# Optimization experiments

Hardware: AMD Instinct MI355X
Metric: run time of the kernel (lower is better)

The kernel has to match this reference:

```python
import jax, jax.numpy as jnp
import numpy as np

ALPHA = 0.2
NOISE_STD = 0.05
I, H, O, R, S, G = 3, 2048, 2, 2, 4, 7
B, T = 32, 512


def _proxies(wi, unitwi, m, n, unitm, unitn, wo, h0, unith0, bias, gb, uv, sup):
    # gb: (G,H) gaussian basis, uv: (1,H) unit vector, sup: (S,H) support masks
    def comb(p, up):  # p: (K,S,G), up: (K,S,1) -> (K,H)
        return jnp.sum((jnp.einsum('ksg,gh->ksh', p, gb) + up * uv) * sup, axis=1)

    wi_full = comb(wi, unitwi)                                          # (I,H)
    m_rec = comb(m, unitm).T                                            # (H,R)
    n_rec = comb(n, unitn).T                                            # (H,R)
    wo_full = jnp.sum(jnp.einsum('osg,gh->osh', wo, gb) * sup, axis=1).T  # (H,O)
    h0_full = jnp.sum((h0 @ gb) * sup, axis=0) + jnp.sum((unith0 * uv) * sup, axis=0)  # (H,)
    bias_full = jnp.sum((bias * uv) * sup, axis=0)                      # (H,)
    w_rec = m_rec @ n_rec.T                                             # (H,H)
    return wi_full, wo_full, w_rec, h0_full, bias_full


def setup_inputs() -> dict:
    key = jax.random.key(0)
    ks = jax.random.split(key, 16)
    sc = 1.0 / np.sqrt(G)
    sup = np.zeros((S, H), dtype=np.float32)
    l = H // S
    for i in range(S):
        sup[i, l * i:l * (i + 1)] = 1.0
    return {
        'input': jax.random.normal(ks[0], (B, T, I), jnp.float32),
        'noise': jax.random.normal(ks[1], (B, T, H), jnp.float32),
        'wi': jax.random.normal(ks[2], (I, S, G), jnp.float32) * sc,
        'unitwi': jax.random.normal(ks[3], (I, S, 1), jnp.float32) * sc,
        'm': jax.random.normal(ks[4], (R, S, G), jnp.float32) * sc,
        'n': jax.random.normal(ks[5], (R, S, G), jnp.float32) * sc,
        'unitm': jax.random.normal(ks[6], (R, S, 1), jnp.float32) * sc,
        'unitn': jax.random.normal(ks[7], (R, S, 1), jnp.float32) * sc,
        'wo': jax.random.normal(ks[8], (O, S, G), jnp.float32) * sc,
        'h0': jax.random.normal(ks[9], (S, G), jnp.float32) * sc,
        'unith0': jax.random.normal(ks[10], (S, 1), jnp.float32) * sc,
        'bias': jax.random.normal(ks[11], (S, 1), jnp.float32) * 0.01,
        'gaussian_basis': jax.random.normal(ks[12], (G, H), jnp.float32),
        'unit_vector': jnp.ones((1, H), jnp.float32),
        'supports': jnp.asarray(sup),
    }


def reference(input, noise, wi, unitwi, m, n, unitm, unitn, wo, h0, unith0, bias,
              gaussian_basis, unit_vector, supports):
    wi_full, wo_full, w_rec, h0_full, bias_full = _proxies(
        wi, unitwi, m, n, unitm, unitn, wo, h0, unith0, bias,
        gaussian_basis, unit_vector, supports)
    batch = input.shape[0]
    h0b = jnp.broadcast_to(h0_full, (batch, h0_full.shape[0]))  # (B,H)

    def step(h, xs):
        x_t, z_t = xs                       # (B,I), (B,H)
        r = jnp.tanh(h)
        h = h + bias_full + NOISE_STD * z_t + ALPHA * (-h + r @ w_rec.T + x_t @ wi_full)
        r = jnp.tanh(h)
        return h, (r @ wo_full, h)

    _, (out, traj) = jax.lax.scan(step, h0b,
                                  (jnp.swapaxes(input, 0, 1), jnp.swapaxes(noise, 0, 1)))
    return jnp.swapaxes(out, 0, 1), jnp.swapaxes(traj, 0, 1)  # (B,T,O), (B,T,H)
```

## Files before the change

### kernel.cpp

```cpp
#include <hip/hip_runtime.h>

typedef float v2f __attribute__((ext_vector_type(2)));

constexpr int I_N = 3, H_N = 2048, O_N = 2, S_N = 4, G_N = 7;
constexpr int B_N = 32, T_N = 512;
constexpr int TPB = 512;
constexpr int EPT = H_N / TPB;
constexpr float ALPHA_C = 0.2f;
constexpr float NSTD_C = 0.05f;
constexpr float TWO_LOG2E = 2.885390081777927f;

__device__ __forceinline__ float fast_tanh(float x) {
  float e = __builtin_amdgcn_exp2f(x * TWO_LOG2E);
  return fmaf(-2.0f, __builtin_amdgcn_rcpf(e + 1.0f), 1.0f);
}

#define DPP_ADD(x, ctrl, rmask)                                                \
  x += __int_as_float(__builtin_amdgcn_update_dpp(                             \
      0, __float_as_int(x), (ctrl), (rmask), 0xf, true))

__device__ __forceinline__ float wave_sum63(float x) {
  DPP_ADD(x, 0x111, 0xf);
  DPP_ADD(x, 0x112, 0xf);
  DPP_ADD(x, 0x114, 0xf);
  DPP_ADD(x, 0x118, 0xf);
  DPP_ADD(x, 0x142, 0xa);
  DPP_ADD(x, 0x143, 0xc);
  return x;
}

__device__ __forceinline__ float rfl(float v) {
  return __int_as_float(__builtin_amdgcn_readfirstlane(__float_as_int(v)));
}

__global__ __launch_bounds__(256) void wo_precomp(
    const float* __restrict__ wo, const float* __restrict__ gb,
    const float* __restrict__ sup, float2* __restrict__ ws2) {
  const int h = blockIdx.x * 256 + threadIdx.x;
  const int s = h >> 9;
  const float sv = sup[s * H_N + h];
  float c0 = 0.f, c1 = 0.f;
#pragma unroll
  for (int g = 0; g < G_N; ++g) {
    const float gv = gb[g * H_N + h];
    c0 = fmaf(wo[(0 * S_N + s) * G_N + g], gv, c0);
    c1 = fmaf(wo[(1 * S_N + s) * G_N + g], gv, c1);
  }
  ws2[h] = make_float2(c0 * sv, c1 * sv);
}

__global__ __launch_bounds__(256) void out_proj(
    const float* __restrict__ traj, const float2* __restrict__ ws2,
    float* __restrict__ out) {
  const int blk = blockIdx.x;
  const int tid = threadIdx.x;
  const int lane = tid & 63;
  const int wave = tid >> 6;
  const int hb = tid * 8;

  __shared__ float2 red[4];

  const float* tp = traj + (size_t)blk * H_N + hb;
  float4 t0 = *(const float4*)tp;
  float4 t1 = *(const float4*)(tp + 4);
  float2 c[8];
#pragma unroll
  for (int e = 0; e < 8; ++e) c[e] = ws2[hb + e];

  float hv[8] = {t0.x, t0.y, t0.z, t0.w, t1.x, t1.y, t1.z, t1.w};
  float p0 = 0.f, p1 = 0.f;
#pragma unroll
  for (int e = 0; e < 8; ++e) {
    const float rv = fast_tanh(hv[e]);
    p0 = fmaf(rv, c[e].x, p0);
    p1 = fmaf(rv, c[e].y, p1);
  }
  p0 = wave_sum63(p0);
  p1 = wave_sum63(p1);
  if (lane == 63) red[wave] = make_float2(p0, p1);
  __syncthreads();
  if (tid == 0) {
    float o0 = 0.f, o1 = 0.f;
#pragma unroll
    for (int w = 0; w < 4; ++w) {
      o0 += red[w].x;
      o1 += red[w].y;
    }
    ((float2*)out)[blk] = make_float2(o0, o1);
  }
}

__global__ __launch_bounds__(TPB) void rnn_fused(
    const float* __restrict__ input,
    const float* __restrict__ noise,
    const float* __restrict__ wi,
    const float* __restrict__ unitwi,
    const float* __restrict__ m_,
    const float* __restrict__ n_,
    const float* __restrict__ unitm,
    const float* __restrict__ unitn,
    const float* __restrict__ h0,
    const float* __restrict__ unith0,
    const float* __restrict__ bias,
    const float* __restrict__ gb,
    const float* __restrict__ uv,
    const float* __restrict__ sup,
    float* __restrict__ traj) {
  const int tid = threadIdx.x;
  const int lane = tid & 63;
  const int wave = tid >> 6;
  const int b = blockIdx.x;
  const int hbase = tid * EPT;
  const int s = hbase >> 9;

  __shared__ float2 parts[2][16];
  __shared__ float4 xs4[T_N];

  float cn0[EPT], cn1[EPT], cm0[EPT], cm1[EPT];
  float cw0[EPT], cw1[EPT], cw2[EPT];
  float cb[EPT], hh_[EPT], r[EPT];

  for (int e = 0; e < EPT; ++e) {
    const int hh = hbase + e;
    float gbh[G_N];
#pragma unroll
    for (int g = 0; g < G_N; ++g) gbh[g] = gb[g * H_N + hh];
    const float uvh = uv[hh];
    const float sv = sup[s * H_N + hh];

    auto comb = [&](const float* p, const float* up, int k) {
      float acc = up[k * S_N + s] * uvh;
#pragma unroll
      for (int g = 0; g < G_N; ++g)
        acc = fmaf(p[(k * S_N + s) * G_N + g], gbh[g], acc);
      return acc * sv;
    };

    cn0[e] = comb(n_, unitn, 0);
    cn1[e] = comb(n_, unitn, 1);
    cm0[e] = ALPHA_C * comb(m_, unitm, 0);
    cm1[e] = ALPHA_C * comb(m_, unitm, 1);
    cw0[e] = ALPHA_C * comb(wi, unitwi, 0);
    cw1[e] = ALPHA_C * comb(wi, unitwi, 1);
    cw2[e] = ALPHA_C * comb(wi, unitwi, 2);
    cb[e] = bias[s] * uvh * sv;
    hh_[e] = comb(h0, unith0, 0);
    r[e] = fast_tanh(hh_[e]);
  }

  v2f cnp[EPT];
  v2f cm0p[2], cm1p[2], cw0p[2], cw1p[2], cw2p[2], cbp[2];
#pragma unroll
  for (int e = 0; e < EPT; ++e) cnp[e] = (v2f){cn0[e], cn1[e]};
#pragma unroll
  for (int p2 = 0; p2 < 2; ++p2) {
    cm0p[p2] = (v2f){cm0[2 * p2], cm0[2 * p2 + 1]};
    cm1p[p2] = (v2f){cm1[2 * p2], cm1[2 * p2 + 1]};
    cw0p[p2] = (v2f){cw0[2 * p2], cw0[2 * p2 + 1]};
    cw1p[p2] = (v2f){cw1[2 * p2], cw1[2 * p2 + 1]};
    cw2p[p2] = (v2f){cw2[2 * p2], cw2[2 * p2 + 1]};
    cbp[p2] = (v2f){cb[2 * p2], cb[2 * p2 + 1]};
  }
  v2f h01 = (v2f){hh_[0], hh_[1]};
  v2f h23 = (v2f){hh_[2], hh_[3]};

  const float* zp = noise + ((size_t)b * T_N) * H_N + hbase;
  const float* xp = input + ((size_t)b * T_N) * I_N;
  float* tp = traj + ((size_t)b * T_N) * H_N + hbase;

  {
    const float* xq = xp + tid * I_N;
    xs4[tid] = make_float4(xq[0], xq[1], xq[2], 0.0f);
  }
  if (tid < 16) parts[tid >> 3][8 + (tid & 7)] = make_float2(0.f, 0.f);

  float4 zr0 = *(const float4*)zp;
  float4 zr1 = *(const float4*)(zp + 1 * (size_t)H_N);
  float4 zr2 = *(const float4*)(zp + 2 * (size_t)H_N);
  float4 zr3 = *(const float4*)(zp + 3 * (size_t)H_N);
  float4 zr4 = *(const float4*)(zp + 4 * (size_t)H_N);
  float4 zr5 = *(const float4*)(zp + 5 * (size_t)H_N);
  float4 zr6 = *(const float4*)(zp + 6 * (size_t)H_N);
  float4 zr7 = *(const float4*)(zp + 7 * (size_t)H_N);

  __builtin_amdgcn_s_waitcnt(0xC07F);
  __builtin_amdgcn_s_barrier();
  __asm__ volatile("" ::: "memory");

  float4 xv = xs4[0];

  auto body = [&](int t, int pb, float4& zslot) {
    const float4 z0 = zslot;
    const int tz = (t + 8 < T_N) ? t + 8 : T_N - 1;
    float4 zn = *(const float4*)(zp + (size_t)tz * H_N);
    const int tx = (t + 1 < T_N) ? t + 1 : T_N - 1;
    float4 xn = xs4[tx];

    v2f z01 = (v2f){z0.x, z0.y}, z23 = (v2f){z0.z, z0.w};
    v2f pre01 = cbp[0];
    pre01 += NSTD_C * z01;
    pre01 += xv.x * cw0p[0];
    pre01 += xv.y * cw1p[0];
    pre01 += xv.z * cw2p[0];
    v2f pre23 = cbp[1];
    pre23 += NSTD_C * z23;
    pre23 += xv.x * cw0p[1];
    pre23 += xv.y * cw1p[1];
    pre23 += xv.z * cw2p[1];

    v2f accA = (v2f){0.f, 0.f};
#pragma unroll
    for (int e = 0; e < EPT; ++e) {
      v2f rr = (v2f){r[e], r[e]};
      accA += rr * cnp[e];
    }
    float pa0 = wave_sum63(accA.x);
    float pa1 = wave_sum63(accA.y);
    if (lane == 63) parts[pb][wave] = make_float2(pa0, pa1);

    __builtin_amdgcn_s_waitcnt(0xC07F);
    __builtin_amdgcn_s_barrier();
    __asm__ volatile("" ::: "memory");

    float2 v = parts[pb][lane & 15];
    DPP_ADD(v.x, 0x101, 0xf); DPP_ADD(v.x, 0x102, 0xf); DPP_ADD(v.x, 0x104, 0xf);
    DPP_ADD(v.y, 0x101, 0xf); DPP_ADD(v.y, 0x102, 0xf); DPP_ADD(v.y, 0x104, 0xf);
    const float a0 = rfl(v.x);
    const float a1 = rfl(v.y);

    h01 = 0.8f * h01 + pre01;
    h01 += a0 * cm0p[0];
    h01 += a1 * cm1p[0];
    h23 = 0.8f * h23 + pre23;
    h23 += a0 * cm0p[1];
    h23 += a1 * cm1p[1];

    *(float4*)(tp + (size_t)t * H_N) = make_float4(h01.x, h01.y, h23.x, h23.y);

    r[0] = fast_tanh(h01.x);
    r[1] = fast_tanh(h01.y);
    r[2] = fast_tanh(h23.x);
    r[3] = fast_tanh(h23.y);

    zslot = zn;
    xv = xn;
  };

  for (int t = 0; t < T_N; t += 8) {
    body(t, 0, zr0);
    body(t + 1, 1, zr1);
    body(t + 2, 0, zr2);
    body(t + 3, 1, zr3);
    body(t + 4, 0, zr4);
    body(t + 5, 1, zr5);
    body(t + 6, 0, zr6);
    body(t + 7, 1, zr7);
  }
}

extern "C" void kernel_launch(void* const* d_in, const int* in_sizes, int n_in,
                              void* d_out, int out_size, void* d_ws, size_t ws_size,
                              hipStream_t stream) {
  const float* input  = (const float*)d_in[0];
  const float* noise  = (const float*)d_in[1];
  const float* wi     = (const float*)d_in[2];
  const float* unitwi = (const float*)d_in[3];
  const float* m_     = (const float*)d_in[4];
  const float* n_     = (const float*)d_in[5];
  const float* unitm  = (const float*)d_in[6];
  const float* unitn  = (const float*)d_in[7];
  const float* wo     = (const float*)d_in[8];
  const float* h0     = (const float*)d_in[9];
  const float* unith0 = (const float*)d_in[10];
  const float* bias   = (const float*)d_in[11];
  const float* gb     = (const float*)d_in[12];
  const float* uv     = (const float*)d_in[13];
  const float* sup    = (const float*)d_in[14];

  float* out  = (float*)d_out;
  float* traj = out + (size_t)B_N * T_N * O_N;
  float2* ws2 = (float2*)d_ws;

  wo_precomp<<<dim3(H_N / 256), dim3(256), 0, stream>>>(wo, gb, sup, ws2);
  rnn_fused<<<dim3(B_N), dim3(TPB), 0, stream>>>(
      input, noise, wi, unitwi, m_, n_, unitm, unitn, h0, unith0, bias,
      gb, uv, sup, traj);
  out_proj<<<dim3(B_N * T_N), dim3(256), 0, stream>>>(traj, ws2, out);
}
```

Baseline: 430.1 us.

## Fuse output projection into recurrent kernel, dropping precompute and projection kernels

The readout r@wo is now computed inside the recurrent kernel. It reuses the tanh values already held for the recurrent matvec and the same wave and cross-wave reduction, with results buffered in shared memory and written once at the end. This removes two extra kernel launches and the out_proj pass, which re-read the whole trajectory from memory. The cost is two more wave reductions per timestep on the serial critical path, plus extra registers.

After: 483.3 us. 12.4% more time.

```diff
diff --git a/kernel.cpp b/kernel.cpp
--- a/kernel.cpp
+++ b/kernel.cpp
@@ -31,63 +31,6 @@
 
 __device__ __forceinline__ float rfl(float v) {
   return __int_as_float(__builtin_amdgcn_readfirstlane(__float_as_int(v)));
-}
-
-__global__ __launch_bounds__(256) void wo_precomp(
-    const float* __restrict__ wo, const float* __restrict__ gb,
-    const float* __restrict__ sup, float2* __restrict__ ws2) {
-  const int h = blockIdx.x * 256 + threadIdx.x;
-  const int s = h >> 9;
-  const float sv = sup[s * H_N + h];
-  float c0 = 0.f, c1 = 0.f;
-#pragma unroll
-  for (int g = 0; g < G_N; ++g) {
-    const float gv = gb[g * H_N + h];
-    c0 = fmaf(wo[(0 * S_N + s) * G_N + g], gv, c0);
-    c1 = fmaf(wo[(1 * S_N + s) * G_N + g], gv, c1);
-  }
-  ws2[h] = make_float2(c0 * sv, c1 * sv);
-}
-
-__global__ __launch_bounds__(256) void out_proj(
-    const float* __restrict__ traj, const float2* __restrict__ ws2,
-    float* __restrict__ out) {
-  const int blk = blockIdx.x;
-  const int tid = threadIdx.x;
-  const int lane = tid & 63;
-  const int wave = tid >> 6;
-  const int hb = tid * 8;
-
-  __shared__ float2 red[4];
-
-  const float* tp = traj + (size_t)blk * H_N + hb;
-  float4 t0 = *(const float4*)tp;
-  float4 t1 = *(const float4*)(tp + 4);
-  float2 c[8];
-#pragma unroll
-  for (int e = 0; e < 8; ++e) c[e] = ws2[hb + e];
-
-  float hv[8] = {t0.x, t0.y, t0.z, t0.w, t1.x, t1.y, t1.z, t1.w};
-  float p0 = 0.f, p1 = 0.f;
-#pragma unroll
-  for (int e = 0; e < 8; ++e) {
-    const float rv = fast_tanh(hv[e]);
-    p0 = fmaf(rv, c[e].x, p0);
-    p1 = fmaf(rv, c[e].y, p1);
-  }
-  p0 = wave_sum63(p0);
-  p1 = wave_sum63(p1);
-  if (lane == 63) red[wave] = make_float2(p0, p1);
-  __syncthreads();
-  if (tid == 0) {
-    float o0 = 0.f, o1 = 0.f;
-#pragma unroll
-    for (int w = 0; w < 4; ++w) {
-      o0 += red[w].x;
-      o1 += red[w].y;
-    }
-    ((float2*)out)[blk] = make_float2(o0, o1);
-  }
 }
 
 __global__ __launch_bounds__(TPB) void rnn_fused(
@@ -99,12 +42,14 @@
     const float* __restrict__ n_,
     const float* __restrict__ unitm,
     const float* __restrict__ unitn,
+    const float* __restrict__ wo,
     const float* __restrict__ h0,
     const float* __restrict__ unith0,
     const float* __restrict__ bias,
     const float* __restrict__ gb,
     const float* __restrict__ uv,
     const float* __restrict__ sup,
+    float* __restrict__ outg,
     float* __restrict__ traj) {
   const int tid = threadIdx.x;
   const int lane = tid & 63;
@@ -113,11 +58,13 @@
   const int hbase = tid * EPT;
   const int s = hbase >> 9;
 
-  __shared__ float2 parts[2][16];
+  __shared__ float4 parts[2][16];
   __shared__ float4 xs4[T_N];
+  __shared__ float2 outb[T_N];
 
   float cn0[EPT], cn1[EPT], cm0[EPT], cm1[EPT];
   float cw0[EPT], cw1[EPT], cw2[EPT];
+  float co0[EPT], co1[EPT];
   float cb[EPT], hh_[EPT], r[EPT];
 
   for (int e = 0; e < EPT; ++e) {
@@ -130,6 +77,13 @@
 
     auto comb = [&](const float* p, const float* up, int k) {
       float acc = up[k * S_N + s] * uvh;
+#pragma unroll
+      for (int g = 0; g < G_N; ++g)
+        acc = fmaf(p[(k * S_N + s) * G_N + g], gbh[g], acc);
+      return acc * sv;
+    };
+    auto combG = [&](const float* p, int k) {
+      float acc = 0.f;
 #pragma unroll
       for (int g = 0; g < G_N; ++g)
         acc = fmaf(p[(k * S_N + s) * G_N + g], gbh[g], acc);
@@ -143,15 +97,20 @@
     cw0[e] = ALPHA_C * comb(wi, unitwi, 0);
     cw1[e] = ALPHA_C * comb(wi, unitwi, 1);
     cw2[e] = ALPHA_C * comb(wi, unitwi, 2);
+    co0[e] = combG(wo, 0);
+    co1[e] = combG(wo, 1);
     cb[e] = bias[s] * uvh * sv;
     hh_[e] = comb(h0, unith0, 0);
     r[e] = fast_tanh(hh_[e]);
   }
 
-  v2f cnp[EPT];
+  v2f cnp[EPT], cop[EPT];
   v2f cm0p[2], cm1p[2], cw0p[2], cw1p[2], cw2p[2], cbp[2];
 #pragma unroll
-  for (int e = 0; e < EPT; ++e) cnp[e] = (v2f){cn0[e], cn1[e]};
+  for (int e = 0; e < EPT; ++e) {
+    cnp[e] = (v2f){cn0[e], cn1[e]};
+    cop[e] = (v2f){co0[e], co1[e]};
+  }
 #pragma unroll
   for (int p2 = 0; p2 < 2; ++p2) {
     cm0p[p2] = (v2f){cm0[2 * p2], cm0[2 * p2 + 1]};
@@ -167,12 +126,13 @@
   const float* zp = noise + ((size_t)b * T_N) * H_N + hbase;
   const float* xp = input + ((size_t)b * T_N) * I_N;
   float* tp = traj + ((size_t)b * T_N) * H_N + hbase;
+  float2* op = (float2*)outg + (size_t)b * T_N;
 
   {
     const float* xq = xp + tid * I_N;
     xs4[tid] = make_float4(xq[0], xq[1], xq[2], 0.0f);
   }
-  if (tid < 16) parts[tid >> 3][8 + (tid & 7)] = make_float2(0.f, 0.f);
+  if (tid < 16) parts[tid >> 3][8 + (tid & 7)] = make_float4(0.f, 0.f, 0.f, 0.f);
 
   float4 zr0 = *(const float4*)zp;
   float4 zr1 = *(const float4*)(zp + 1 * (size_t)H_N);
@@ -189,7 +149,7 @@
 
   float4 xv = xs4[0];
 
-  auto body = [&](int t, int pb, float4& zslot) {
+  auto body = [&](int t, int pbuf, float4& zslot) {
     const float4 z0 = zslot;
     const int tz = (t + 8 < T_N) ? t + 8 : T_N - 1;
     float4 zn = *(const float4*)(zp + (size_t)tz * H_N);
@@ -209,24 +169,33 @@
     pre23 += xv.z * cw2p[1];
 
     v2f accA = (v2f){0.f, 0.f};
+    v2f accO = (v2f){0.f, 0.f};
 #pragma unroll
     for (int e = 0; e < EPT; ++e) {
       v2f rr = (v2f){r[e], r[e]};
       accA += rr * cnp[e];
+      accO += rr * cop[e];
     }
     float pa0 = wave_sum63(accA.x);
     float pa1 = wave_sum63(accA.y);
-    if (lane == 63) parts[pb][wave] = make_float2(pa0, pa1);
+    float po0 = wave_sum63(accO.x);
+    float po1 = wave_sum63(accO.y);
+    if (lane == 63) parts[pbuf][wave] = make_float4(pa0, pa1, po0, po1);
 
     __builtin_amdgcn_s_waitcnt(0xC07F);
     __builtin_amdgcn_s_barrier();
     __asm__ volatile("" ::: "memory");
 
-    float2 v = parts[pb][lane & 15];
+    float4 v = parts[pbuf][lane & 15];
     DPP_ADD(v.x, 0x101, 0xf); DPP_ADD(v.x, 0x102, 0xf); DPP_ADD(v.x, 0x104, 0xf);
     DPP_ADD(v.y, 0x101, 0xf); DPP_ADD(v.y, 0x102, 0xf); DPP_ADD(v.y, 0x104, 0xf);
     const float a0 = rfl(v.x);
     const float a1 = rfl(v.y);
+    if (wave == 0) {
+      DPP_ADD(v.z, 0x101, 0xf); DPP_ADD(v.z, 0x102, 0xf); DPP_ADD(v.z, 0x104, 0xf);
+      DPP_ADD(v.w, 0x101, 0xf); DPP_ADD(v.w, 0x102, 0xf); DPP_ADD(v.w, 0x104, 0xf);
+      if (lane == 0 && t > 0) outb[t - 1] = make_float2(v.z, v.w);
+    }
 
     h01 = 0.8f * h01 + pre01;
     h01 += a0 * cm0p[0];
@@ -255,6 +224,27 @@
     body(t + 5, 1, zr5);
     body(t + 6, 0, zr6);
     body(t + 7, 1, zr7);
+  }
+
+  {
+    v2f accO = (v2f){0.f, 0.f};
+#pragma unroll
+    for (int e = 0; e < EPT; ++e) {
+      v2f rr = (v2f){r[e], r[e]};
+      accO += rr * cop[e];
+    }
+    float po0 = wave_sum63(accO.x);
+    float po1 = wave_sum63(accO.y);
+    if (lane == 63) parts[0][wave] = make_float4(po0, po1, 0.f, 0.f);
+    __syncthreads();
+    if (wave == 0) {
+      float4 v = parts[0][lane & 15];
+      DPP_ADD(v.x, 0x101, 0xf); DPP_ADD(v.x, 0x102, 0xf); DPP_ADD(v.x, 0x104, 0xf);
+      DPP_ADD(v.y, 0x101, 0xf); DPP_ADD(v.y, 0x102, 0xf); DPP_ADD(v.y, 0x104, 0xf);
+      if (lane == 0) outb[T_N - 1] = make_float2(v.x, v.y);
+    }
+    __syncthreads();
+    op[tid] = outb[tid];
   }
 }
 
@@ -279,11 +269,8 @@
 
   float* out  = (float*)d_out;
   float* traj = out + (size_t)B_N * T_N * O_N;
-  float2* ws2 = (float2*)d_ws;
-
-  wo_precomp<<<dim3(H_N / 256), dim3(256), 0, stream>>>(wo, gb, sup, ws2);
+
   rnn_fused<<<dim3(B_N), dim3(TPB), 0, stream>>>(
-      input, noise, wi, unitwi, m_, n_, unitm, unitn, h0, unith0, bias,
-      gb, uv, sup, traj);
-  out_proj<<<dim3(B_N * T_N), dim3(256), 0, stream>>>(traj, ws2, out);
-}
+      input, noise, wi, unitwi, m_, n_, unitm, unitn, wo, h0, unith0, bias,
+      gb, uv, sup, out, traj);
+}
```

## Halve recurrent block to 256 threads with 8 elements per thread

Applied to the files above, without the earlier changes.

Cuts the recurrent kernel from 512 to 256 threads, so each thread handles 8 hidden units and there are only 4 waves per block. The cross-wave reduction becomes two float4 LDS reads plus adds, replacing the DPP tree and readfirstlane, which shortens the critical path on every serial time step. Noise prefetch depth drops from 8 steps to 4 and loads are split into two float4s per step. The trade is more per-thread ALU work per step and less latency hiding for the noise stream.

Result: slower. 468.6 us (+8.9%).

```diff
diff --git a/kernel.cpp b/kernel.cpp
--- a/kernel.cpp
+++ b/kernel.cpp
@@ -4,7 +4,7 @@
 
 constexpr int I_N = 3, H_N = 2048, O_N = 2, S_N = 4, G_N = 7;
 constexpr int B_N = 32, T_N = 512;
-constexpr int TPB = 512;
+constexpr int TPB = 256;
 constexpr int EPT = H_N / TPB;
 constexpr float ALPHA_C = 0.2f;
 constexpr float NSTD_C = 0.05f;
@@ -27,10 +27,6 @@
   DPP_ADD(x, 0x142, 0xa);
   DPP_ADD(x, 0x143, 0xc);
   return x;
-}
-
-__device__ __forceinline__ float rfl(float v) {
-  return __int_as_float(__builtin_amdgcn_readfirstlane(__float_as_int(v)));
 }
 
 __global__ __launch_bounds__(256) void wo_precomp(
@@ -113,7 +109,7 @@
   const int hbase = tid * EPT;
   const int s = hbase >> 9;
 
-  __shared__ float2 parts[2][16];
+  __shared__ float4 partsq[2][2];
   __shared__ float4 xs4[T_N];
 
   float cn0[EPT], cn1[EPT], cm0[EPT], cm1[EPT];
@@ -149,20 +145,20 @@
   }
 
   v2f cnp[EPT];
-  v2f cm0p[2], cm1p[2], cw0p[2], cw1p[2], cw2p[2], cbp[2];
+  v2f cm0p[EPT / 2], cm1p[EPT / 2], cw0p[EPT / 2], cw1p[EPT / 2],
+      cw2p[EPT / 2], cbp[EPT / 2], hp[EPT / 2];
 #pragma unroll
   for (int e = 0; e < EPT; ++e) cnp[e] = (v2f){cn0[e], cn1[e]};
 #pragma unroll
-  for (int p2 = 0; p2 < 2; ++p2) {
+  for (int p2 = 0; p2 < EPT / 2; ++p2) {
     cm0p[p2] = (v2f){cm0[2 * p2], cm0[2 * p2 + 1]};
     cm1p[p2] = (v2f){cm1[2 * p2], cm1[2 * p2 + 1]};
     cw0p[p2] = (v2f){cw0[2 * p2], cw0[2 * p2 + 1]};
     cw1p[p2] = (v2f){cw1[2 * p2], cw1[2 * p2 + 1]};
     cw2p[p2] = (v2f){cw2[2 * p2], cw2[2 * p2 + 1]};
     cbp[p2] = (v2f){cb[2 * p2], cb[2 * p2 + 1]};
-  }
-  v2f h01 = (v2f){hh_[0], hh_[1]};
-  v2f h23 = (v2f){hh_[2], hh_[3]};
+    hp[p2] = (v2f){hh_[2 * p2], hh_[2 * p2 + 1]};
+  }
 
   const float* zp = noise + ((size_t)b * T_N) * H_N + hbase;
   const float* xp = input + ((size_t)b * T_N) * I_N;
@@ -171,17 +167,18 @@
   {
     const float* xq = xp + tid * I_N;
     xs4[tid] = make_float4(xq[0], xq[1], xq[2], 0.0f);
-  }
-  if (tid < 16) parts[tid >> 3][8 + (tid & 7)] = make_float2(0.f, 0.f);
-
-  float4 zr0 = *(const float4*)zp;
-  float4 zr1 = *(const float4*)(zp + 1 * (size_t)H_N);
-  float4 zr2 = *(const float4*)(zp + 2 * (size_t)H_N);
-  float4 zr3 = *(const float4*)(zp + 3 * (size_t)H_N);
-  float4 zr4 = *(const float4*)(zp + 4 * (size_t)H_N);
-  float4 zr5 = *(const float4*)(zp + 5 * (size_t)H_N);
-  float4 zr6 = *(const float4*)(zp + 6 * (size_t)H_N);
-  float4 zr7 = *(const float4*)(zp + 7 * (size_t)H_N);
+    const float* xq2 = xp + (tid + 256) * I_N;
+    xs4[tid + 256] = make_float4(xq2[0], xq2[1], xq2[2], 0.0f);
+  }
+
+  float4 zA0 = *(const float4*)zp;
+  float4 zB0 = *(const float4*)(zp + 4);
+  float4 zA1 = *(const float4*)(zp + 1 * (size_t)H_N);
+  float4 zB1 = *(const float4*)(zp + 1 * (size_t)H_N + 4);
+  float4 zA2 = *(const float4*)(zp + 2 * (size_t)H_N);
+  float4 zB2 = *(const float4*)(zp + 2 * (size_t)H_N + 4);
+  float4 zA3 = *(const float4*)(zp + 3 * (size_t)H_N);
+  float4 zB3 = *(const float4*)(zp + 3 * (size_t)H_N + 4);
 
   __builtin_amdgcn_s_waitcnt(0xC07F);
   __builtin_amdgcn_s_barrier();
@@ -189,72 +186,81 @@
 
   float4 xv = xs4[0];
 
-  auto body = [&](int t, int pb, float4& zslot) {
-    const float4 z0 = zslot;
-    const int tz = (t + 8 < T_N) ? t + 8 : T_N - 1;
-    float4 zn = *(const float4*)(zp + (size_t)tz * H_N);
+  auto body = [&](int t, int pbuf, float4& zsA, float4& zsB) {
+    const float4 za = zsA;
+    const float4 zb = zsB;
+    const int tz = (t + 4 < T_N) ? t + 4 : T_N - 1;
+    float4 znA = *(const float4*)(zp + (size_t)tz * H_N);
+    float4 znB = *(const float4*)(zp + (size_t)tz * H_N + 4);
     const int tx = (t + 1 < T_N) ? t + 1 : T_N - 1;
     float4 xn = xs4[tx];
 
-    v2f z01 = (v2f){z0.x, z0.y}, z23 = (v2f){z0.z, z0.w};
-    v2f pre01 = cbp[0];
-    pre01 += NSTD_C * z01;
-    pre01 += xv.x * cw0p[0];
-    pre01 += xv.y * cw1p[0];
-    pre01 += xv.z * cw2p[0];
-    v2f pre23 = cbp[1];
-    pre23 += NSTD_C * z23;
-    pre23 += xv.x * cw0p[1];
-    pre23 += xv.y * cw1p[1];
-    pre23 += xv.z * cw2p[1];
-
-    v2f accA = (v2f){0.f, 0.f};
-#pragma unroll
-    for (int e = 0; e < EPT; ++e) {
-      v2f rr = (v2f){r[e], r[e]};
-      accA += rr * cnp[e];
-    }
+    v2f zpk[4] = {(v2f){za.x, za.y}, (v2f){za.z, za.w},
+                  (v2f){zb.x, zb.y}, (v2f){zb.z, zb.w}};
+    v2f pre[4];
+#pragma unroll
+    for (int p2 = 0; p2 < 4; ++p2) {
+      v2f acc = cbp[p2];
+      acc += NSTD_C * zpk[p2];
+      acc += xv.x * cw0p[p2];
+      acc += xv.y * cw1p[p2];
+      acc += xv.z * cw2p[p2];
+      pre[p2] = acc;
+    }
+
+    v2f accE = (v2f){0.f, 0.f};
+    v2f accD = (v2f){0.f, 0.f};
+#pragma unroll
+    for (int e = 0; e < EPT; e += 2) {
+      accE += (v2f){r[e], r[e]} * cnp[e];
+      accD += (v2f){r[e + 1], r[e + 1]} * cnp[e + 1];
+    }
+    v2f accA = accE + accD;
     float pa0 = wave_sum63(accA.x);
     float pa1 = wave_sum63(accA.y);
-    if (lane == 63) parts[pb][wave] = make_float2(pa0, pa1);
+    if (lane == 63)
+      ((float2*)&partsq[pbuf][0])[wave] = make_float2(pa0, pa1);
 
     __builtin_amdgcn_s_waitcnt(0xC07F);
     __builtin_amdgcn_s_barrier();
     __asm__ volatile("" ::: "memory");
 
-    float2 v = parts[pb][lane & 15];
-    DPP_ADD(v.x, 0x101, 0xf); DPP_ADD(v.x, 0x102, 0xf); DPP_ADD(v.x, 0x104, 0xf);
-    DPP_ADD(v.y, 0x101, 0xf); DPP_ADD(v.y, 0x102, 0xf); DPP_ADD(v.y, 0x104, 0xf);
-    const float a0 = rfl(v.x);
-    const float a1 = rfl(v.y);
-
-    h01 = 0.8f * h01 + pre01;
-    h01 += a0 * cm0p[0];
-    h01 += a1 * cm1p[0];
-    h23 = 0.8f * h23 + pre23;
-    h23 += a0 * cm0p[1];
-    h23 += a1 * cm1p[1];
-
-    *(float4*)(tp + (size_t)t * H_N) = make_float4(h01.x, h01.y, h23.x, h23.y);
-
-    r[0] = fast_tanh(h01.x);
-    r[1] = fast_tanh(h01.y);
-    r[2] = fast_tanh(h23.x);
-    r[3] = fast_tanh(h23.y);
-
-    zslot = zn;
+    const float4 q0 = partsq[pbuf][0];
+    const float4 q1 = partsq[pbuf][1];
+    v2f u = ((v2f){q0.x, q0.y} + (v2f){q0.z, q0.w}) +
+            ((v2f){q1.x, q1.y} + (v2f){q1.z, q1.w});
+    const float a0 = u.x;
+    const float a1 = u.y;
+
+#pragma unroll
+    for (int p2 = 0; p2 < 4; ++p2) {
+      v2f hv = 0.8f * hp[p2] + pre[p2];
+      hv += a0 * cm0p[p2];
+      hv += a1 * cm1p[p2];
+      hp[p2] = hv;
+    }
+
+    *(float4*)(tp + (size_t)t * H_N) =
+        make_float4(hp[0].x, hp[0].y, hp[1].x, hp[1].y);
+    *(float4*)(tp + (size_t)t * H_N + 4) =
+        make_float4(hp[2].x, hp[2].y, hp[3].x, hp[3].y);
+
+#pragma unroll
+    for (int p2 = 0; p2 < 4; ++p2) {
+      r[2 * p2] = fast_tanh(hp[p2].x);
+      r[2 * p2 + 1] = fast_tanh(hp[p2].y);
+    }
+
+    zsA = znA;
+    zsB = znB;
     xv = xn;
   };
 
-  for (int t = 0; t < T_N; t += 8) {
-    body(t, 0, zr0);
-    body(t + 1, 1, zr1);
-    body(t + 2, 0, zr2);
-    body(t + 3, 1, zr3);
-    body(t + 4, 0, zr4);
-    body(t + 5, 1, zr5);
-    body(t + 6, 0, zr6);
-    body(t + 7, 1, zr7);
+  for (int t = 0; t < T_N; t += 4) {
+    body(t, 0, zA0, zB0);
+    body(t + 1, 1, zA1, zB1);
+    body(t + 2, 0, zA2, zB2);
+    body(t + 3, 1, zA3, zB3);
   }
 }
 
```

## Replace per-step workgroup barrier with LDS atomic counters and fold tanh algebra

Applied to the files above, without the earlier changes.

Replaces the s_barrier in each recurrence step with a per-slot LDS atomic counter that waves increment after publishing their partial sums, then spin on until all eight arrive, using four rotating slots. Also rewrites tanh(h)=1-2/(1+e) so the constant part of the r·n product is precomputed and only the reciprocal term is multiplied each step. The aim is to let waves proceed without a full barrier and shave ALU work on the serial critical path, at the cost of spin-wait polling traffic on LDS.

Measured after the change: 456.2 us. 1.06x slower.

```diff
diff --git a/kernel.cpp b/kernel.cpp
--- a/kernel.cpp
+++ b/kernel.cpp
@@ -113,12 +113,13 @@
   const int hbase = tid * EPT;
   const int s = hbase >> 9;
 
-  __shared__ float2 parts[2][16];
+  __shared__ float2 parts[4][16];
+  __shared__ unsigned done_cnt[4];
   __shared__ float4 xs4[T_N];
 
   float cn0[EPT], cn1[EPT], cm0[EPT], cm1[EPT];
   float cw0[EPT], cw1[EPT], cw2[EPT];
-  float cb[EPT], hh_[EPT], r[EPT];
+  float cb[EPT], hh_[EPT];
 
   for (int e = 0; e < EPT; ++e) {
     const int hh = hbase + e;
@@ -145,13 +146,21 @@
     cw2[e] = ALPHA_C * comb(wi, unitwi, 2);
     cb[e] = bias[s] * uvh * sv;
     hh_[e] = comb(h0, unith0, 0);
-    r[e] = fast_tanh(hh_[e]);
-  }
-
-  v2f cnp[EPT];
+  }
+
+  v2f c2n[EPT];
+  v2f cnsE, cnsD;
   v2f cm0p[2], cm1p[2], cw0p[2], cw1p[2], cw2p[2], cbp[2];
-#pragma unroll
-  for (int e = 0; e < EPT; ++e) cnp[e] = (v2f){cn0[e], cn1[e]};
+  {
+    v2f cnp[EPT];
+#pragma unroll
+    for (int e = 0; e < EPT; ++e) {
+      cnp[e] = (v2f){cn0[e], cn1[e]};
+      c2n[e] = -2.0f * cnp[e];
+    }
+    cnsE = cnp[0] + cnp[2];
+    cnsD = cnp[1] + cnp[3];
+  }
 #pragma unroll
   for (int p2 = 0; p2 < 2; ++p2) {
     cm0p[p2] = (v2f){cm0[2 * p2], cm0[2 * p2 + 1]};
@@ -163,6 +172,17 @@
   }
   v2f h01 = (v2f){hh_[0], hh_[1]};
   v2f h23 = (v2f){hh_[2], hh_[3]};
+  v2f w01, w23;
+  {
+    float e0 = __builtin_amdgcn_exp2f(h01.x * TWO_LOG2E);
+    float e1 = __builtin_amdgcn_exp2f(h01.y * TWO_LOG2E);
+    float e2 = __builtin_amdgcn_exp2f(h23.x * TWO_LOG2E);
+    float e3 = __builtin_amdgcn_exp2f(h23.y * TWO_LOG2E);
+    w01 = (v2f){__builtin_amdgcn_rcpf(e0 + 1.0f),
+                __builtin_amdgcn_rcpf(e1 + 1.0f)};
+    w23 = (v2f){__builtin_amdgcn_rcpf(e2 + 1.0f),
+                __builtin_amdgcn_rcpf(e3 + 1.0f)};
+  }
 
   const float* zp = noise + ((size_t)b * T_N) * H_N + hbase;
   const float* xp = input + ((size_t)b * T_N) * I_N;
@@ -172,7 +192,8 @@
     const float* xq = xp + tid * I_N;
     xs4[tid] = make_float4(xq[0], xq[1], xq[2], 0.0f);
   }
-  if (tid < 16) parts[tid >> 3][8 + (tid & 7)] = make_float2(0.f, 0.f);
+  if (tid < 4) done_cnt[tid] = 0u;
+  if (tid < 32) parts[tid >> 3][8 + (tid & 7)] = make_float2(0.f, 0.f);
 
   float4 zr0 = *(const float4*)zp;
   float4 zr1 = *(const float4*)(zp + 1 * (size_t)H_N);
@@ -189,7 +210,7 @@
 
   float4 xv = xs4[0];
 
-  auto body = [&](int t, int pb, float4& zslot) {
+  auto body = [&](int t, int slot, unsigned tgt, float4& zslot) {
     const float4 z0 = zslot;
     const int tz = (t + 8 < T_N) ? t + 8 : T_N - 1;
     float4 zn = *(const float4*)(zp + (size_t)tz * H_N);
@@ -208,21 +229,31 @@
     pre23 += xv.y * cw1p[1];
     pre23 += xv.z * cw2p[1];
 
-    v2f accA = (v2f){0.f, 0.f};
-#pragma unroll
-    for (int e = 0; e < EPT; ++e) {
-      v2f rr = (v2f){r[e], r[e]};
-      accA += rr * cnp[e];
-    }
+    v2f accE = cnsE;
+    accE += w01.x * c2n[0];
+    accE += w23.x * c2n[2];
+    v2f accD = cnsD;
+    accD += w01.y * c2n[1];
+    accD += w23.y * c2n[3];
+    v2f accA = accE + accD;
     float pa0 = wave_sum63(accA.x);
     float pa1 = wave_sum63(accA.y);
-    if (lane == 63) parts[pb][wave] = make_float2(pa0, pa1);
-
-    __builtin_amdgcn_s_waitcnt(0xC07F);
-    __builtin_amdgcn_s_barrier();
+
+    if (lane == 63) {
+      parts[slot][wave] = make_float2(pa0, pa1);
+      __asm__ volatile("" ::: "memory");
+      __builtin_amdgcn_s_waitcnt(0xC07F);
+      __asm__ volatile("" ::: "memory");
+      __hip_atomic_fetch_add(&done_cnt[slot], 1u, __ATOMIC_RELEASE,
+                             __HIP_MEMORY_SCOPE_WORKGROUP);
+    }
+
+    while (__hip_atomic_load(&done_cnt[slot], __ATOMIC_ACQUIRE,
+                             __HIP_MEMORY_SCOPE_WORKGROUP) < tgt) {
+    }
     __asm__ volatile("" ::: "memory");
 
-    float2 v = parts[pb][lane & 15];
+    float2 v = parts[slot][lane & 15];
     DPP_ADD(v.x, 0x101, 0xf); DPP_ADD(v.x, 0x102, 0xf); DPP_ADD(v.x, 0x104, 0xf);
     DPP_ADD(v.y, 0x101, 0xf); DPP_ADD(v.y, 0x102, 0xf); DPP_ADD(v.y, 0x104, 0xf);
     const float a0 = rfl(v.x);
@@ -237,24 +268,30 @@
 
     *(float4*)(tp + (size_t)t * H_N) = make_float4(h01.x, h01.y, h23.x, h23.y);
 
-    r[0] = fast_tanh(h01.x);
-    r[1] = fast_tanh(h01.y);
-    r[2] = fast_tanh(h23.x);
-    r[3] = fast_tanh(h23.y);
+    float e0 = __builtin_amdgcn_exp2f(h01.x * TWO_LOG2E);
+    float e1 = __builtin_amdgcn_exp2f(h01.y * TWO_LOG2E);
+    float e2 = __builtin_amdgcn_exp2f(h23.x * TWO_LOG2E);
+    float e3 = __builtin_amdgcn_exp2f(h23.y * TWO_LOG2E);
+    w01 = (v2f){__builtin_amdgcn_rcpf(e0 + 1.0f),
+                __builtin_amdgcn_rcpf(e1 + 1.0f)};
+    w23 = (v2f){__builtin_amdgcn_rcpf(e2 + 1.0f),
+                __builtin_amdgcn_rcpf(e3 + 1.0f)};
 
     zslot = zn;
     xv = xn;
   };
 
   for (int t = 0; t < T_N; t += 8) {
-    body(t, 0, zr0);
-    body(t + 1, 1, zr1);
-    body(t + 2, 0, zr2);
-    body(t + 3, 1, zr3);
-    body(t + 4, 0, zr4);
-    body(t + 5, 1, zr5);
-    body(t + 6, 0, zr6);
-    body(t + 7, 1, zr7);
+    const unsigned tg0 = (unsigned)(2 * t) + 8u;
+    const unsigned tg1 = tg0 + 8u;
+    body(t,     0, tg0, zr0);
+    body(t + 1, 1, tg0, zr1);
+    body(t + 2, 2, tg0, zr2);
+    body(t + 3, 3, tg0, zr3);
+    body(t + 4, 0, tg1, zr4);
+    body(t + 5, 1, tg1, zr5);
+    body(t + 6, 2, tg1, zr6);
+    body(t + 7, 3, tg1, zr7);
   }
 }
 
```
